# Kernel tuning notes

Measured on AMD Instinct MI355X. Metric: run time of the kernel, lower is better.

Reference implementation:

```python
import jax, jax.numpy as jnp
import numpy as np

LAM = 0.5
LAG = 1
ALPHA = 0.5
EPS = 1e-8


def setup_inputs() -> dict:
    key = jax.random.key(0)
    k1, k2, k3, k4 = jax.random.split(key, 4)
    B, T, F, H = 64, 4096, 64, 256
    return {
        "input": jax.random.normal(k1, (B, T, 1), dtype=jnp.float32),
        "target": jax.random.normal(k2, (B, T, 1), dtype=jnp.float32),
        "sequence": jax.random.normal(k3, (B, T, F), dtype=jnp.float32),
        "forget_gates": jax.random.uniform(k4, (B, T, H), dtype=jnp.float32),
    }


def reference(input, target, sequence, forget_gates):
    B, T, F = sequence.shape
    x = jnp.moveaxis(sequence, 1, 0)          # [T, B, F] time-major
    x_t = x[LAG:]                              # [T-LAG, B, F]
    x_lag = x[:-LAG]                           # [T-LAG, B, F]

    m0 = jnp.zeros((B, F), dtype=sequence.dtype)
    v0 = jnp.full((B, F), EPS, dtype=sequence.dtype)
    c0 = jnp.zeros((B, F), dtype=sequence.dtype)

    def step(carry, inp):
        m, v, c = carry
        xt, xl = inp
        m = LAM * m + (1.0 - LAM) * xt
        v = LAM * v + (1.0 - LAM) * (xt - m) ** 2
        c = LAM * c + (1.0 - LAM) * (xt - m) * (xl - m)
        ac = c / jnp.sqrt(v * v + EPS)         # matches torch: sqrt(var*var + eps)
        return (m, v, c), ac

    _, acs = jax.lax.scan(step, (m0, v0, c0), (x_t, x_lag))  # [T-LAG, B, F]
    pad = jnp.zeros((LAG, B, F), dtype=sequence.dtype)       # initial_padding zeros
    ac_full = jnp.concatenate([pad, acs], axis=0)            # [T, B, F]

    irrelevance = 1.0 - jnp.abs(ac_full)                     # [T, B, F]
    irrelevance = jnp.mean(irrelevance, axis=2, keepdims=True)  # [T, B, 1]
    irrelevance = jnp.moveaxis(irrelevance, 0, 1)            # [B, T, 1]

    penalty = jnp.mean(irrelevance * forget_gates)
    mse = jnp.mean((input - target) ** 2)
    return mse + ALPHA * penalty
```

## Files before the change

### kernel.cpp

```cpp
#include <hip/hip_runtime.h>

constexpr int B = 64;
constexpr int T = 4096;
constexpr int F = 64;
constexpr int H = 256;
constexpr float EPSC = 1e-8f;
constexpr float ALPHAC = 0.5f;

constexpr int C = 128;
constexpr int W = 48;
constexpr int CHUNKS = T / C;

constexpr int K0_BLOCKS = 2048;
constexpr int K1_BLOCKS = (B * CHUNKS) / 4;

#define WS_FGSUM 0
#define WS_MSE   (B * T)
#define WS_PEN   (B * T + K0_BLOCKS)

__global__ __launch_bounds__(256) void k_rowsum_mse(
    const float* __restrict__ fg,
    const float* __restrict__ inp,
    const float* __restrict__ tgt,
    float* __restrict__ ws) {
  float* fgsum = ws + WS_FGSUM;
  const int lane = threadIdx.x & 63;
  const int wave = (blockIdx.x * blockDim.x + threadIdx.x) >> 6;
  const int nwaves = (gridDim.x * blockDim.x) >> 6;
  const int R = B * T;

  for (int r = wave; r < R; r += nwaves) {
    const float4 q = *reinterpret_cast<const float4*>(fg + (size_t)r * H + lane * 4);
    float s = (q.x + q.y) + (q.z + q.w);
#pragma unroll
    for (int off = 32; off; off >>= 1) s += __shfl_xor(s, off, 64);
    if (lane == 0) fgsum[r] = s;
  }

  float acc = 0.f;
  const int tid = blockIdx.x * blockDim.x + threadIdx.x;
  const int nt = gridDim.x * blockDim.x;
  for (int i = tid; i < R; i += nt) {
    float d = inp[i] - tgt[i];
    acc = fmaf(d, d, acc);
  }
#pragma unroll
  for (int off = 32; off; off >>= 1) acc += __shfl_xor(acc, off, 64);
  __shared__ float sm[4];
  if ((threadIdx.x & 63) == 0) sm[threadIdx.x >> 6] = acc;
  __syncthreads();
  if (threadIdx.x == 0)
    ws[WS_MSE + blockIdx.x] = (sm[0] + sm[1]) + (sm[2] + sm[3]);
}

__global__ __launch_bounds__(256) void k_scan(
    const float* __restrict__ seq,
    float* __restrict__ ws) {
  const float* fgsum = ws + WS_FGSUM;
  const int lane = threadIdx.x & 63;
  const int task = blockIdx.x * (blockDim.x >> 6) + (threadIdx.x >> 6);
  const int b = task / CHUNKS;
  const int ci = task % CHUNKS;
  const int t0 = ci * C;

  const float* sp = seq + (size_t)b * T * F + lane;
  const float* fp = fgsum + (size_t)b * T;

  float m = 0.f, v = 0.f, c = 0.f;
  float acc = 0.f;
  float xl;
  int t;

  if (ci == 0) {
    v = EPSC;
    acc = fp[0];
    xl = sp[0];
    t = 1;
  } else {
    const int ts = t0 - W;
    xl = sp[(ts - 1) * F];
    for (t = ts; t < t0; ++t) {
      const float xt = sp[t * F];
      m = 0.5f * (m + xt);
      const float d = xt - m;
      v = 0.5f * fmaf(d, d, v);
      c = 0.5f * fmaf(d, xl - m, c);
      xl = xt;
    }
  }

  const int tend = t0 + C;
  for (; t < tend; ++t) {
    const float xt = sp[t * F];
    const float g = fp[t];
    m = 0.5f * (m + xt);
    const float d = xt - m;
    v = 0.5f * fmaf(d, d, v);
    c = 0.5f * fmaf(d, xl - m, c);
    const float ac = c * rsqrtf(fmaf(v, v, EPSC));
    acc = fmaf(1.0f - fabsf(ac), g, acc);
    xl = xt;
  }

#pragma unroll
  for (int off = 32; off; off >>= 1) acc += __shfl_xor(acc, off, 64);
  if (lane == 0) ws[WS_PEN + task] = acc;
}

__global__ __launch_bounds__(256) void k_reduce(
    const float* __restrict__ ws,
    float* __restrict__ out) {
  float m = 0.f, p = 0.f;
#pragma unroll
  for (int i = 0; i < K0_BLOCKS / 256; ++i)
    m += ws[WS_MSE + threadIdx.x + i * 256];
#pragma unroll
  for (int i = 0; i < 2048 / 256; ++i)
    p += ws[WS_PEN + threadIdx.x + i * 256];
#pragma unroll
  for (int off = 32; off; off >>= 1) {
    m += __shfl_xor(m, off, 64);
    p += __shfl_xor(p, off, 64);
  }
  __shared__ float sm[8];
  if ((threadIdx.x & 63) == 0) {
    sm[(threadIdx.x >> 6) * 2]     = m;
    sm[(threadIdx.x >> 6) * 2 + 1] = p;
  }
  __syncthreads();
  if (threadIdx.x == 0) {
    float mt = sm[0] + sm[2] + sm[4] + sm[6];
    float pt = sm[1] + sm[3] + sm[5] + sm[7];
    const float R = (float)B * (float)T;
    const float pscale = ALPHAC / (R * (float)H * (float)F);
    out[0] = mt / R + pt * pscale;
  }
}

extern "C" void kernel_launch(void* const* d_in, const int* in_sizes, int n_in,
                              void* d_out, int out_size, void* d_ws, size_t ws_size,
                              hipStream_t stream) {
  const float* inp = (const float*)d_in[0];
  const float* tgt = (const float*)d_in[1];
  const float* seq = (const float*)d_in[2];
  const float* fg  = (const float*)d_in[3];
  float* out = (float*)d_out;
  float* ws  = (float*)d_ws;

  k_rowsum_mse<<<K0_BLOCKS, 256, 0, stream>>>(fg, inp, tgt, ws);
  k_scan<<<K1_BLOCKS, 256, 0, stream>>>(seq, ws);
  k_reduce<<<1, 256, 0, stream>>>(ws, out);
}
```

Before: 446.4 us.

## Fuse forget-gate row sums and MSE into the scan kernel with prefetching

Merges the forget-gate row-sum/MSE kernel into the chunked scan kernel. Each wave now reads its own forget-gate rows directly and reduces them with shuffles, so the intermediate B*T row-sum array is no longer written and re-read. A 4-deep register prefetch ring is added for the sequence and gate loads, and the warm-up loop is fully unrolled. The cost is extra shuffle work inside the serial scan loop, and the scan now waits on forget-gate memory latency on its critical path.

```diff
diff --git a/kernel.cpp b/kernel.cpp
--- a/kernel.cpp
+++ b/kernel.cpp
@@ -10,77 +10,43 @@
 constexpr int C = 128;
 constexpr int W = 48;
 constexpr int CHUNKS = T / C;
+constexpr int NTASK = B * CHUNKS;
+constexpr int K_BLOCKS = NTASK / 4;
 
-constexpr int K0_BLOCKS = 2048;
-constexpr int K1_BLOCKS = (B * CHUNKS) / 4;
+#define WS_PEN 0
+#define WS_MSE NTASK
 
-#define WS_FGSUM 0
-#define WS_MSE   (B * T)
-#define WS_PEN   (B * T + K0_BLOCKS)
-
-__global__ __launch_bounds__(256) void k_rowsum_mse(
+__global__ __launch_bounds__(256) void k_fused(
+    const float* __restrict__ seq,
     const float* __restrict__ fg,
     const float* __restrict__ inp,
     const float* __restrict__ tgt,
     float* __restrict__ ws) {
-  float* fgsum = ws + WS_FGSUM;
-  const int lane = threadIdx.x & 63;
-  const int wave = (blockIdx.x * blockDim.x + threadIdx.x) >> 6;
-  const int nwaves = (gridDim.x * blockDim.x) >> 6;
-  const int R = B * T;
-
-  for (int r = wave; r < R; r += nwaves) {
-    const float4 q = *reinterpret_cast<const float4*>(fg + (size_t)r * H + lane * 4);
-    float s = (q.x + q.y) + (q.z + q.w);
-#pragma unroll
-    for (int off = 32; off; off >>= 1) s += __shfl_xor(s, off, 64);
-    if (lane == 0) fgsum[r] = s;
-  }
-
-  float acc = 0.f;
-  const int tid = blockIdx.x * blockDim.x + threadIdx.x;
-  const int nt = gridDim.x * blockDim.x;
-  for (int i = tid; i < R; i += nt) {
-    float d = inp[i] - tgt[i];
-    acc = fmaf(d, d, acc);
-  }
-#pragma unroll
-  for (int off = 32; off; off >>= 1) acc += __shfl_xor(acc, off, 64);
-  __shared__ float sm[4];
-  if ((threadIdx.x & 63) == 0) sm[threadIdx.x >> 6] = acc;
-  __syncthreads();
-  if (threadIdx.x == 0)
-    ws[WS_MSE + blockIdx.x] = (sm[0] + sm[1]) + (sm[2] + sm[3]);
-}
-
-__global__ __launch_bounds__(256) void k_scan(
-    const float* __restrict__ seq,
-    float* __restrict__ ws) {
-  const float* fgsum = ws + WS_FGSUM;
   const int lane = threadIdx.x & 63;
   const int task = blockIdx.x * (blockDim.x >> 6) + (threadIdx.x >> 6);
   const int b = task / CHUNKS;
   const int ci = task % CHUNKS;
   const int t0 = ci * C;
+  const int tend = t0 + C;
 
   const float* sp = seq + (size_t)b * T * F + lane;
-  const float* fp = fgsum + (size_t)b * T;
+  const float* gp = fg + (size_t)b * T * H + lane * 4;
 
-  float m = 0.f, v = 0.f, c = 0.f;
-  float acc = 0.f;
-  float xl;
-  int t;
+  float m = 0.f, v = 0.f, c = 0.f, acc = 0.f;
+  float xl = 0.f;
 
   if (ci == 0) {
     v = EPSC;
-    acc = fp[0];
-    xl = sp[0];
-    t = 1;
   } else {
     const int ts = t0 - W;
     xl = sp[(ts - 1) * F];
-    for (t = ts; t < t0; ++t) {
-      const float xt = sp[t * F];
+    float xw[4];
+#pragma unroll
+    for (int j = 0; j < 4; ++j) xw[j] = sp[(ts + j) * F];
+#pragma unroll
+    for (int i = 0; i < W; ++i) {
+      const float xt = xw[i & 3];
+      if (i + 4 < W) xw[i & 3] = sp[(ts + i + 4) * F];
       m = 0.5f * (m + xt);
       const float d = xt - m;
       v = 0.5f * fmaf(d, d, v);
@@ -89,51 +55,90 @@
     }
   }
 
-  const int tend = t0 + C;
-  for (; t < tend; ++t) {
-    const float xt = sp[t * F];
-    const float g = fp[t];
-    m = 0.5f * (m + xt);
-    const float d = xt - m;
-    v = 0.5f * fmaf(d, d, v);
-    c = 0.5f * fmaf(d, xl - m, c);
-    const float ac = c * rsqrtf(fmaf(v, v, EPSC));
-    acc = fmaf(1.0f - fabsf(ac), g, acc);
+  const int tstart = t0;
+  float4 qb[4];
+  float xb[4];
+#pragma unroll
+  for (int j = 0; j < 4; ++j) {
+    qb[j] = *reinterpret_cast<const float4*>(gp + (size_t)(tstart + j) * H);
+    xb[j] = sp[(tstart + j) * F];
+  }
+
+#pragma unroll 4
+  for (int i = 0; i < C; ++i) {
+    const int tt = tstart + i;
+    const float4 q = qb[i & 3];
+    const float xt = xb[i & 3];
+    int tp = tt + 4;
+    tp = (tp < tend) ? tp : (tend - 1);
+    qb[i & 3] = *reinterpret_cast<const float4*>(gp + (size_t)tp * H);
+    xb[i & 3] = sp[tp * F];
+
+    float s = (q.x + q.y) + (q.z + q.w);
+#pragma unroll
+    for (int off = 32; off; off >>= 1) s += __shfl_xor(s, off, 64);
+
+    if (tt != 0) {
+      m = 0.5f * (m + xt);
+      const float d = xt - m;
+      v = 0.5f * fmaf(d, d, v);
+      c = 0.5f * fmaf(d, xl - m, c);
+      const float ac = c * rsqrtf(fmaf(v, v, EPSC));
+      acc = fmaf(1.0f - fabsf(ac), s, acc);
+    } else {
+      acc += s;
+    }
     xl = xt;
   }
 
 #pragma unroll
   for (int off = 32; off; off >>= 1) acc += __shfl_xor(acc, off, 64);
   if (lane == 0) ws[WS_PEN + task] = acc;
+
+  float macc = 0.f;
+  const int gid = blockIdx.x * blockDim.x + threadIdx.x;
+  const int nt = gridDim.x * blockDim.x;
+  const int R = B * T;
+  for (int i = gid; i < R; i += nt) {
+    const float d = inp[i] - tgt[i];
+    macc = fmaf(d, d, macc);
+  }
+#pragma unroll
+  for (int off = 32; off; off >>= 1) macc += __shfl_xor(macc, off, 64);
+  __shared__ float sm[4];
+  if ((threadIdx.x & 63) == 0) sm[threadIdx.x >> 6] = macc;
+  __syncthreads();
+  if (threadIdx.x == 0)
+    ws[WS_MSE + blockIdx.x] = (sm[0] + sm[1]) + (sm[2] + sm[3]);
 }
 
 __global__ __launch_bounds__(256) void k_reduce(
     const float* __restrict__ ws,
     float* __restrict__ out) {
-  float m = 0.f, p = 0.f;
+  float p = 0.f, mt = 0.f;
 #pragma unroll
-  for (int i = 0; i < K0_BLOCKS / 256; ++i)
-    m += ws[WS_MSE + threadIdx.x + i * 256];
-#pragma unroll
-  for (int i = 0; i < 2048 / 256; ++i)
+  for (int i = 0; i < NTASK / 256; ++i)
     p += ws[WS_PEN + threadIdx.x + i * 256];
 #pragma unroll
+  for (int i = 0; i < K_BLOCKS / 256; ++i)
+    mt += ws[WS_MSE + threadIdx.x + i * 256];
+#pragma unroll
   for (int off = 32; off; off >>= 1) {
-    m += __shfl_xor(m, off, 64);
     p += __shfl_xor(p, off, 64);
+    mt += __shfl_xor(mt, off, 64);
   }
   __shared__ float sm[8];
   if ((threadIdx.x & 63) == 0) {
-    sm[(threadIdx.x >> 6) * 2]     = m;
-    sm[(threadIdx.x >> 6) * 2 + 1] = p;
+    sm[(threadIdx.x >> 6) * 2] = p;
+    sm[(threadIdx.x >> 6) * 2 + 1] = mt;
   }
   __syncthreads();
   if (threadIdx.x == 0) {
-    float mt = sm[0] + sm[2] + sm[4] + sm[6];
-    float pt = sm[1] + sm[3] + sm[5] + sm[7];
+    const float pt = sm[0] + sm[2] + sm[4] + sm[6];
+    const float ms = sm[1] + sm[3] + sm[5] + sm[7];
     const float R = (float)B * (float)T;
     const float pscale = ALPHAC / (R * (float)H * (float)F);
-    out[0] = mt / R + pt * pscale;
+    out[0] = ms / R + pt * pscale;
   }
 }
 
@@ -147,7 +152,6 @@
   float* out = (float*)d_out;
   float* ws  = (float*)d_ws;
 
-  k_rowsum_mse<<<K0_BLOCKS, 256, 0, stream>>>(fg, inp, tgt, ws);
-  k_scan<<<K1_BLOCKS, 256, 0, stream>>>(seq, ws);
+  k_fused<<<K_BLOCKS, 256, 0, stream>>>(seq, fg, inp, tgt, ws);
   k_reduce<<<1, 256, 0, stream>>>(ws, out);
 }
```

After: 407.3 us. -8.8%, faster.
